# Performance work log

Hardware: AMD Instinct MI355X
Metric: run time of the kernel (lower is better)

Reference implementation:

```python
import jax, jax.numpy as jnp
import numpy as np

B, H, NQ, NL, NA = 262144, 256, 4, 2, 16


def _apply_1q(s, U, q):
    # s: [B, 2,2,2,2]; U: [B,2,2] (batched) or [2,2] (shared)
    s = jnp.moveaxis(s, 1 + q, -1)
    if U.ndim == 3:
        s = jnp.einsum('bij,b...j->b...i', U, s)
    else:
        s = jnp.einsum('ij,b...j->b...i', U, s)
    return jnp.moveaxis(s, -1, 1 + q)


def _apply_cnot(s, c, t):
    s = jnp.moveaxis(s, (1 + c, 1 + t), (-2, -1))
    s = jnp.stack([s[..., 0, :], s[..., 1, ::-1]], axis=-2)  # flip target when control=1
    return jnp.moveaxis(s, (-2, -1), (1 + c, 1 + t))


def _rx(theta):
    # batched RX: theta [B] -> [B,2,2]
    c = jnp.cos(theta / 2).astype(jnp.complex64)
    s = (-1j) * jnp.sin(theta / 2)
    return jnp.stack([jnp.stack([c, s], -1), jnp.stack([s, c], -1)], -2)


def _rot(phi, theta, omega):
    # PennyLane Rot = RZ(omega) @ RY(theta) @ RZ(phi), scalar angles -> [2,2]
    c, s = jnp.cos(theta / 2), jnp.sin(theta / 2)
    return jnp.array(1, jnp.complex64) * jnp.stack([
        jnp.stack([jnp.exp(-0.5j * (phi + omega)) * c, -jnp.exp(0.5j * (phi - omega)) * s], -1),
        jnp.stack([jnp.exp(-0.5j * (phi - omega)) * s, jnp.exp(0.5j * (phi + omega)) * c], -1),
    ], -2)


def _circuit(angles, q_weights):
    # angles: [B, NQ] -> PauliZ expvals [B, NQ] via 4-qubit state-vector sim
    b = angles.shape[0]
    s = jnp.zeros((b,) + (2,) * NQ, jnp.complex64)
    s = s.at[(slice(None),) + (0,) * NQ].set(1.0)
    for q in range(NQ):  # AngleEmbedding (RX rotations)
        s = _apply_1q(s, _rx(angles[:, q]), q)
    for l in range(NL):  # StronglyEntanglingLayers
        for w in range(NQ):
            s = _apply_1q(s, _rot(q_weights[l, w, 0], q_weights[l, w, 1], q_weights[l, w, 2]), w)
        r = l % (NQ - 1) + 1
        for w in range(NQ):
            s = _apply_cnot(s, w, (w + r) % NQ)
    probs = s.real ** 2 + s.imag ** 2  # [B,2,2,2,2]
    zs = []
    axes = tuple(range(1, NQ + 1))
    for q in range(NQ):
        p = probs.sum(tuple(a for a in axes if a != 1 + q))  # [B,2]
        zs.append(p[:, 0] - p[:, 1])
    return jnp.stack(zs, axis=1)


def setup_inputs() -> dict:
    key = jax.random.key(0)
    ks = jax.random.split(key, 6)
    return {
        'h': jax.random.normal(ks[0], (B, H), jnp.float32),
        'W_embed': jax.random.normal(ks[1], (NQ, H), jnp.float32) / np.sqrt(H),
        'b_embed': jnp.zeros((NQ,), jnp.float32),
        'q_weights': jax.random.uniform(ks[2], (NL, NQ, 3), jnp.float32, 0.0, 2 * np.pi),
        'W_out': jax.random.normal(ks[3], (NA, NQ), jnp.float32) / np.sqrt(NQ),
        'b_out': jnp.zeros((NA,), jnp.float32),
    }


def reference(h, W_embed, b_embed, q_weights, W_out, b_out):
    angles = jnp.tanh(h @ W_embed.T + b_embed)  # [B, NQ]
    z = _circuit(angles, q_weights)             # [B, NQ]
    return z @ W_out.T + b_out                  # [B, NA]
```

## Files before the change

### kernel.cpp

```cpp
#include <hip/hip_runtime.h>

#define NQ 4
#define NL 2
#define NA 16
#define HDIM 256
#define RPB 256

template<int M>
__device__ __forceinline__ void apply_u(float* sr, float* si, const float* u) {
    const float u00r = u[0], u00i = u[1], u01r = u[2], u01i = u[3];
    const float u10r = u[4], u10i = u[5], u11r = u[6], u11i = u[7];
#pragma unroll
    for (int k = 0; k < 16; ++k) {
        if (k & M) continue;
        const int k1 = k | M;
        const float a0r = sr[k],  a0i = si[k];
        const float a1r = sr[k1], a1i = si[k1];
        sr[k]  = u00r*a0r - u00i*a0i + u01r*a1r - u01i*a1i;
        si[k]  = u00r*a0i + u00i*a0r + u01r*a1i + u01i*a1r;
        sr[k1] = u10r*a0r - u10i*a0i + u11r*a1r - u11i*a1i;
        si[k1] = u10r*a0i + u10i*a0r + u11r*a1i + u11i*a1r;
    }
}

template<int MC, int MT>
__device__ __forceinline__ void cnot(float* sr, float* si) {
#pragma unroll
    for (int k = 0; k < 16; ++k) {
        if ((k & MC) && !(k & MT)) {
            const int k1 = k | MT;
            float tr = sr[k]; sr[k] = sr[k1]; sr[k1] = tr;
            float ti = si[k]; si[k] = si[k1]; si[k1] = ti;
        }
    }
}

__global__ __launch_bounds__(256) void qph_kernel(
    const float* __restrict__ h,
    const float* __restrict__ W_embed,
    const float* __restrict__ b_embed,
    const float* __restrict__ q_weights,
    const float* __restrict__ W_out,
    const float* __restrict__ b_out,
    float* __restrict__ out,
    int B)
{
    __shared__ __align__(16) float w_lds[NQ * HDIM];
    __shared__ float ang_lds[NQ][RPB];
    __shared__ float rot_lds[NL * NQ][8];
    __shared__ float wout_lds[NA * NQ];
    __shared__ float bout_lds[NA];

    const int tid = threadIdx.x;
    const long rowBase = (long)blockIdx.x * RPB;

#pragma unroll
    for (int k = 0; k < 4; ++k) w_lds[tid + k * 256] = W_embed[tid + k * 256];
    if (tid < NA * NQ) wout_lds[tid] = W_out[tid];
    if (tid < NA)      bout_lds[tid] = b_out[tid];
    if (tid < NL * NQ) {
        const float phi = q_weights[tid * 3 + 0];
        const float th  = q_weights[tid * 3 + 1];
        const float om  = q_weights[tid * 3 + 2];
        const float c  = cosf(0.5f * th), s  = sinf(0.5f * th);
        const float al = 0.5f * (phi + om), be = 0.5f * (phi - om);
        const float ca = cosf(al), sa = sinf(al);
        const float cb = cosf(be), sb = sinf(be);
        rot_lds[tid][0] =  ca * c;  rot_lds[tid][1] = -sa * c;
        rot_lds[tid][2] = -cb * s;  rot_lds[tid][3] = -sb * s;
        rot_lds[tid][4] =  cb * s;  rot_lds[tid][5] = -sb * s;
        rot_lds[tid][6] =  ca * c;  rot_lds[tid][7] =  sa * c;
    }
    __syncthreads();

    const int t = tid & 3;
    const int g = tid >> 2;
    const float be0 = b_embed[0], be1 = b_embed[1], be2 = b_embed[2], be3 = b_embed[3];

#pragma unroll
    for (int rr = 0; rr < 4; ++rr) {
        const int  lrow = g * 4 + rr;
        const long grow = rowBase + lrow;
        float acc0 = 0.f, acc1 = 0.f, acc2 = 0.f, acc3 = 0.f;
        if (grow < B) {
            const float4* hrow = (const float4*)(h + grow * (long)HDIM);
#pragma unroll
            for (int j = 0; j < 16; ++j) {
                const float4 hv = hrow[j * 4 + t];
                const float4 w0 = *(const float4*)&w_lds[0 * HDIM + j * 16 + t * 4];
                const float4 w1 = *(const float4*)&w_lds[1 * HDIM + j * 16 + t * 4];
                const float4 w2 = *(const float4*)&w_lds[2 * HDIM + j * 16 + t * 4];
                const float4 w3 = *(const float4*)&w_lds[3 * HDIM + j * 16 + t * 4];
                acc0 = fmaf(hv.x, w0.x, fmaf(hv.y, w0.y, fmaf(hv.z, w0.z, fmaf(hv.w, w0.w, acc0))));
                acc1 = fmaf(hv.x, w1.x, fmaf(hv.y, w1.y, fmaf(hv.z, w1.z, fmaf(hv.w, w1.w, acc1))));
                acc2 = fmaf(hv.x, w2.x, fmaf(hv.y, w2.y, fmaf(hv.z, w2.z, fmaf(hv.w, w2.w, acc2))));
                acc3 = fmaf(hv.x, w3.x, fmaf(hv.y, w3.y, fmaf(hv.z, w3.z, fmaf(hv.w, w3.w, acc3))));
            }
        }
        acc0 += __shfl_xor(acc0, 1); acc0 += __shfl_xor(acc0, 2);
        acc1 += __shfl_xor(acc1, 1); acc1 += __shfl_xor(acc1, 2);
        acc2 += __shfl_xor(acc2, 1); acc2 += __shfl_xor(acc2, 2);
        acc3 += __shfl_xor(acc3, 1); acc3 += __shfl_xor(acc3, 2);
        if (t == 0 && grow < B) {
            ang_lds[0][lrow] = tanhf(acc0 + be0);
            ang_lds[1][lrow] = tanhf(acc1 + be1);
            ang_lds[2][lrow] = tanhf(acc2 + be2);
            ang_lds[3][lrow] = tanhf(acc3 + be3);
        }
    }
    __syncthreads();

    const int  lrow = tid;
    const long grow = rowBase + lrow;
    if (grow >= B) return;

    float sr[16], si[16];
#pragma unroll
    for (int k = 0; k < 16; ++k) { sr[k] = 0.f; si[k] = 0.f; }
    sr[0] = 1.0f;

#pragma unroll
    for (int q = 0; q < NQ; ++q) {
        const float th = ang_lds[q][lrow];
        const float c = __cosf(0.5f * th), s = __sinf(0.5f * th);
        const int m = 8 >> q;
#pragma unroll
        for (int k = 0; k < 16; ++k) {
            if (k & m) continue;
            const int k1 = k | m;
            const float a0r = sr[k],  a0i = si[k];
            const float a1r = sr[k1], a1i = si[k1];
            sr[k]  = c * a0r + s * a1i;
            si[k]  = c * a0i - s * a1r;
            sr[k1] = s * a0i + c * a1r;
            si[k1] = c * a1i - s * a0r;
        }
    }

    apply_u<8>(sr, si, rot_lds[0]);
    apply_u<4>(sr, si, rot_lds[1]);
    apply_u<2>(sr, si, rot_lds[2]);
    apply_u<1>(sr, si, rot_lds[3]);
    cnot<8, 4>(sr, si);
    cnot<4, 2>(sr, si);
    cnot<2, 1>(sr, si);
    cnot<1, 8>(sr, si);
    apply_u<8>(sr, si, rot_lds[4]);
    apply_u<4>(sr, si, rot_lds[5]);
    apply_u<2>(sr, si, rot_lds[6]);
    apply_u<1>(sr, si, rot_lds[7]);
    cnot<8, 2>(sr, si);
    cnot<4, 1>(sr, si);
    cnot<2, 8>(sr, si);
    cnot<1, 4>(sr, si);

    float p[16];
#pragma unroll
    for (int k = 0; k < 16; ++k) p[k] = sr[k] * sr[k] + si[k] * si[k];
    float z[4];
#pragma unroll
    for (int q = 0; q < NQ; ++q) {
        const int m = 8 >> q;
        float zz = 0.f;
#pragma unroll
        for (int k = 0; k < 16; ++k) zz += (k & m) ? -p[k] : p[k];
        z[q] = zz;
    }

    float4* out4 = (float4*)(out + grow * (long)NA);
#pragma unroll
    for (int i = 0; i < 4; ++i) {
        float o[4];
#pragma unroll
        for (int jj = 0; jj < 4; ++jj) {
            const int a = i * 4 + jj;
            float v = bout_lds[a];
#pragma unroll
            for (int q = 0; q < NQ; ++q) v = fmaf(z[q], wout_lds[a * 4 + q], v);
            o[jj] = v;
        }
        out4[i] = make_float4(o[0], o[1], o[2], o[3]);
    }
}

extern "C" void kernel_launch(void* const* d_in, const int* in_sizes, int n_in,
                              void* d_out, int out_size, void* d_ws, size_t ws_size,
                              hipStream_t stream) {
    const float* h         = (const float*)d_in[0];
    const float* W_embed   = (const float*)d_in[1];
    const float* b_embed   = (const float*)d_in[2];
    const float* q_weights = (const float*)d_in[3];
    const float* W_out     = (const float*)d_in[4];
    const float* b_out     = (const float*)d_in[5];
    float* out = (float*)d_out;

    const int B = in_sizes[0] / HDIM;
    const int blocks = (B + RPB - 1) / RPB;
    qph_kernel<<<blocks, 256, 0, stream>>>(h, W_embed, b_embed, q_weights, W_out, b_out, out, B);
}
```

Baseline: 59.05 us.

## Halve rows per block and batch h loads for more memory parallelism

Each block now handles 128 rows instead of 256, so every group of four threads computes two rows at once. It issues 16 float4 global loads per half before the FMAs, raising the number of loads in flight, and a launch-bounds occupancy hint is added. Only half the threads run the quantum-circuit phase, which leaves half the wave idle there. The register pressure from the batched loads may limit occupancy, and the W_embed tile is reloaded into LDS twice as often across the grid.

```diff
diff --git a/kernel.cpp b/kernel.cpp
--- a/kernel.cpp
+++ b/kernel.cpp
@@ -4,7 +4,7 @@
 #define NL 2
 #define NA 16
 #define HDIM 256
-#define RPB 256
+#define RPB 128
 
 template<int M>
 __device__ __forceinline__ void apply_u(float* sr, float* si, const float* u) {
@@ -35,7 +35,7 @@
     }
 }
 
-__global__ __launch_bounds__(256) void qph_kernel(
+__global__ __launch_bounds__(256, 4) void qph_kernel(
     const float* __restrict__ h,
     const float* __restrict__ W_embed,
     const float* __restrict__ b_embed,
@@ -75,44 +75,67 @@
 
     const int t = tid & 3;
     const int g = tid >> 2;
+    const long row0 = rowBase + g * 2;
+    const long row1 = row0 + 1;
     const float be0 = b_embed[0], be1 = b_embed[1], be2 = b_embed[2], be3 = b_embed[3];
 
-#pragma unroll
-    for (int rr = 0; rr < 4; ++rr) {
-        const int  lrow = g * 4 + rr;
-        const long grow = rowBase + lrow;
-        float acc0 = 0.f, acc1 = 0.f, acc2 = 0.f, acc3 = 0.f;
-        if (grow < B) {
-            const float4* hrow = (const float4*)(h + grow * (long)HDIM);
-#pragma unroll
-            for (int j = 0; j < 16; ++j) {
-                const float4 hv = hrow[j * 4 + t];
-                const float4 w0 = *(const float4*)&w_lds[0 * HDIM + j * 16 + t * 4];
-                const float4 w1 = *(const float4*)&w_lds[1 * HDIM + j * 16 + t * 4];
-                const float4 w2 = *(const float4*)&w_lds[2 * HDIM + j * 16 + t * 4];
-                const float4 w3 = *(const float4*)&w_lds[3 * HDIM + j * 16 + t * 4];
-                acc0 = fmaf(hv.x, w0.x, fmaf(hv.y, w0.y, fmaf(hv.z, w0.z, fmaf(hv.w, w0.w, acc0))));
-                acc1 = fmaf(hv.x, w1.x, fmaf(hv.y, w1.y, fmaf(hv.z, w1.z, fmaf(hv.w, w1.w, acc1))));
-                acc2 = fmaf(hv.x, w2.x, fmaf(hv.y, w2.y, fmaf(hv.z, w2.z, fmaf(hv.w, w2.w, acc2))));
-                acc3 = fmaf(hv.x, w3.x, fmaf(hv.y, w3.y, fmaf(hv.z, w3.z, fmaf(hv.w, w3.w, acc3))));
-            }
-        }
-        acc0 += __shfl_xor(acc0, 1); acc0 += __shfl_xor(acc0, 2);
-        acc1 += __shfl_xor(acc1, 1); acc1 += __shfl_xor(acc1, 2);
-        acc2 += __shfl_xor(acc2, 1); acc2 += __shfl_xor(acc2, 2);
-        acc3 += __shfl_xor(acc3, 1); acc3 += __shfl_xor(acc3, 2);
-        if (t == 0 && grow < B) {
-            ang_lds[0][lrow] = tanhf(acc0 + be0);
-            ang_lds[1][lrow] = tanhf(acc1 + be1);
-            ang_lds[2][lrow] = tanhf(acc2 + be2);
-            ang_lds[3][lrow] = tanhf(acc3 + be3);
-        }
+    float acc0[NQ] = {0.f, 0.f, 0.f, 0.f};
+    float acc1[NQ] = {0.f, 0.f, 0.f, 0.f};
+
+    const float4* hr0 = (const float4*)(h + row0 * (long)HDIM);
+    const float4* hr1 = (const float4*)(h + row1 * (long)HDIM);
+
+#pragma unroll
+    for (int half = 0; half < 2; ++half) {
+        const int jb = half * 8;
+        float4 a0[8], a1[8];
+        if (row0 < B) {
+#pragma unroll
+            for (int j = 0; j < 8; ++j) a0[j] = hr0[(jb + j) * 4 + t];
+#pragma unroll
+            for (int j = 0; j < 8; ++j) a1[j] = hr1[(jb + j) * 4 + t];
+        } else {
+#pragma unroll
+            for (int j = 0; j < 8; ++j) { a0[j] = make_float4(0,0,0,0); a1[j] = a0[j]; }
+        }
+#pragma unroll
+        for (int j = 0; j < 8; ++j) {
+            const int col = (jb + j) * 16 + t * 4;
+            const float4 w0 = *(const float4*)&w_lds[0 * HDIM + col];
+            const float4 w1 = *(const float4*)&w_lds[1 * HDIM + col];
+            const float4 w2 = *(const float4*)&w_lds[2 * HDIM + col];
+            const float4 w3 = *(const float4*)&w_lds[3 * HDIM + col];
+            acc0[0] = fmaf(a0[j].x, w0.x, fmaf(a0[j].y, w0.y, fmaf(a0[j].z, w0.z, fmaf(a0[j].w, w0.w, acc0[0]))));
+            acc0[1] = fmaf(a0[j].x, w1.x, fmaf(a0[j].y, w1.y, fmaf(a0[j].z, w1.z, fmaf(a0[j].w, w1.w, acc0[1]))));
+            acc0[2] = fmaf(a0[j].x, w2.x, fmaf(a0[j].y, w2.y, fmaf(a0[j].z, w2.z, fmaf(a0[j].w, w2.w, acc0[2]))));
+            acc0[3] = fmaf(a0[j].x, w3.x, fmaf(a0[j].y, w3.y, fmaf(a0[j].z, w3.z, fmaf(a0[j].w, w3.w, acc0[3]))));
+            acc1[0] = fmaf(a1[j].x, w0.x, fmaf(a1[j].y, w0.y, fmaf(a1[j].z, w0.z, fmaf(a1[j].w, w0.w, acc1[0]))));
+            acc1[1] = fmaf(a1[j].x, w1.x, fmaf(a1[j].y, w1.y, fmaf(a1[j].z, w1.z, fmaf(a1[j].w, w1.w, acc1[1]))));
+            acc1[2] = fmaf(a1[j].x, w2.x, fmaf(a1[j].y, w2.y, fmaf(a1[j].z, w2.z, fmaf(a1[j].w, w2.w, acc1[2]))));
+            acc1[3] = fmaf(a1[j].x, w3.x, fmaf(a1[j].y, w3.y, fmaf(a1[j].z, w3.z, fmaf(a1[j].w, w3.w, acc1[3]))));
+        }
+    }
+
+#pragma unroll
+    for (int q = 0; q < NQ; ++q) {
+        acc0[q] += __shfl_xor(acc0[q], 1); acc0[q] += __shfl_xor(acc0[q], 2);
+        acc1[q] += __shfl_xor(acc1[q], 1); acc1[q] += __shfl_xor(acc1[q], 2);
+    }
+    if (t == 0 && row0 < B) {
+        ang_lds[0][g * 2] = tanhf(acc0[0] + be0);
+        ang_lds[1][g * 2] = tanhf(acc0[1] + be1);
+        ang_lds[2][g * 2] = tanhf(acc0[2] + be2);
+        ang_lds[3][g * 2] = tanhf(acc0[3] + be3);
+        ang_lds[0][g * 2 + 1] = tanhf(acc1[0] + be0);
+        ang_lds[1][g * 2 + 1] = tanhf(acc1[1] + be1);
+        ang_lds[2][g * 2 + 1] = tanhf(acc1[2] + be2);
+        ang_lds[3][g * 2 + 1] = tanhf(acc1[3] + be3);
     }
     __syncthreads();
 
     const int  lrow = tid;
     const long grow = rowBase + lrow;
-    if (grow >= B) return;
+    if (lrow >= RPB || grow >= B) return;
 
     float sr[16], si[16];
 #pragma unroll
```

Result: slower. 174.2 us (+194.9%).
